# Optimization experiments

Measured on AMD Instinct MI355X. Metric: run time of the kernel, lower is better.

## Reference

```python
import jax, jax.numpy as jnp
import numpy as np

REG_PARAM = 0.0002
COS_EPS = 1e-8  # torch F.cosine_similarity eps


def setup_inputs() -> dict:
    key = jax.random.key(0)
    k1, k2, k3, k4 = jax.random.split(key, 4)
    return {
        "output": jax.random.normal(k1, (32, 3, 256, 256), dtype=jnp.float32),
        "ground_truth": jax.random.normal(k2, (32, 3, 256, 256), dtype=jnp.float32),
        "att": jax.random.normal(k3, (8192, 2000), dtype=jnp.float32),
        "mem": jax.random.normal(k4, (2000, 256), dtype=jnp.float32),
    }


def reference(output, ground_truth, att, mem):
    # MSE reconstruction loss (mean reduction)
    mse = jnp.mean((ground_truth - output) ** 2)

    # Entropy regularizer: sum(softmax * log_softmax) over att, dim=1
    logp = jax.nn.log_softmax(att, axis=1)
    reg = jnp.sum(jnp.exp(logp) * logp)
    loss = mse - REG_PARAM * reg

    # Pairwise cosine-similarity sum over memory vectors:
    # original: nested loop over all i<j pairs; here: normalize + Gram + triu sum
    norms = jnp.maximum(jnp.linalg.norm(mem, axis=1, keepdims=True), COS_EPS)
    unit = mem / norms                      # [N, D]
    gram = unit @ unit.T                    # [N, N]
    cos_sum = jnp.sum(jnp.triu(gram, k=1))  # strict upper triangle = i<j pairs

    return loss + cos_sum
```

## Files before the change

kernel.cpp:

```cpp
#include <hip/hip_runtime.h>
#include <math.h>

#define REG_PARAM 0.0002f
#define COS_EPS 1e-8f

#define MSE_BLOCKS 1024
#define ENT_BLOCKS 1024
#define MEM_BLOCKS 64
#define TOTAL_BLOCKS (MSE_BLOCKS + ENT_BLOCKS + MEM_BLOCKS)

#define WS_MSE  0
#define WS_ENT  1024
#define WS_DIAG 2048
#define WS_COL  2112

__device__ __forceinline__ float waveReduceSum(float v) {
    #pragma unroll
    for (int off = 32; off > 0; off >>= 1)
        v += __shfl_xor(v, off, 64);
    return v;
}

__device__ __forceinline__ float blockReduceSum(float v, float* sh) {
    v = waveReduceSum(v);
    int wid = threadIdx.x >> 6, lane = threadIdx.x & 63;
    __syncthreads();
    if (lane == 0) sh[wid] = v;
    __syncthreads();
    return sh[0] + sh[1] + sh[2] + sh[3];
}

__global__ void partials_kernel(const float4* __restrict__ out4,
                                const float4* __restrict__ gt4,
                                const float4* __restrict__ att4,
                                const float4* __restrict__ mem4,
                                float* __restrict__ ws, int n4) {
    __shared__ float sh[4 * 256];
    __shared__ float shd[4];
    const int b = blockIdx.x;
    const int t = threadIdx.x;
    const int wid = t >> 6, lane = t & 63;

    if (b < MSE_BLOCKS) {
        float acc = 0.f;
        for (int i = b * 256 + t; i < n4; i += MSE_BLOCKS * 256) {
            float4 a = out4[i], g = gt4[i];
            float d0 = g.x - a.x, d1 = g.y - a.y;
            float d2 = g.z - a.z, d3 = g.w - a.w;
            acc += d0 * d0 + d1 * d1 + d2 * d2 + d3 * d3;
        }
        acc = waveReduceSum(acc);
        if (lane == 0) sh[wid] = acc;
        __syncthreads();
        if (t == 0) ws[WS_MSE + b] = sh[0] + sh[1] + sh[2] + sh[3];
    } else if (b < MSE_BLOCKS + ENT_BLOCKS) {
        const int wglobal = (b - MSE_BLOCKS) * 4 + wid;
        float acc = 0.f;
        for (int row = wglobal; row < 8192; row += ENT_BLOCKS * 4) {
            const float4* __restrict__ rp = att4 + (size_t)row * 500;
            float z = 0.f, tt = 0.f;
            #pragma unroll
            for (int k = 0; k < 8; ++k) {
                int idx = lane + (k << 6);
                if (idx < 500) {
                    float4 x = rp[idx];
                    float e;
                    e = __expf(x.x); z += e; tt += x.x * e;
                    e = __expf(x.y); z += e; tt += x.y * e;
                    e = __expf(x.z); z += e; tt += x.z * e;
                    e = __expf(x.w); z += e; tt += x.w * e;
                }
            }
            z = waveReduceSum(z);
            tt = waveReduceSum(tt);
            acc += tt / z - __logf(z);
        }
        if (lane == 0) sh[wid] = acc;
        __syncthreads();
        if (t == 0) ws[WS_ENT + (b - MSE_BLOCKS)] = sh[0] + sh[1] + sh[2] + sh[3];
    } else {
        const int mb = b - MSE_BLOCKS - ENT_BLOCKS;
        const int wglobal = mb * 4 + wid;
        float c0 = 0.f, c1 = 0.f, c2 = 0.f, c3 = 0.f, dacc = 0.f;
        for (int row = wglobal; row < 2000; row += 256) {
            float4 v = mem4[(size_t)row * 64 + lane];
            float ss = v.x * v.x + v.y * v.y + v.z * v.z + v.w * v.w;
            ss = waveReduceSum(ss);
            float inv = 1.f / fmaxf(sqrtf(ss), COS_EPS);
            c0 += v.x * inv; c1 += v.y * inv; c2 += v.z * inv; c3 += v.w * inv;
            if (lane == 0) dacc += ss * inv * inv;
        }
        if (lane == 0) shd[wid] = dacc;
        sh[wid * 256 + lane * 4 + 0] = c0;
        sh[wid * 256 + lane * 4 + 1] = c1;
        sh[wid * 256 + lane * 4 + 2] = c2;
        sh[wid * 256 + lane * 4 + 3] = c3;
        __syncthreads();
        ws[WS_COL + mb * 256 + t] = sh[t] + sh[256 + t] + sh[512 + t] + sh[768 + t];
        if (t == 0) ws[WS_DIAG + mb] = shd[0] + shd[1] + shd[2] + shd[3];
    }
}

__global__ void finalize_kernel(const float* __restrict__ ws,
                                float* __restrict__ out, float inv_n) {
    __shared__ float sh[4];
    const int t = threadIdx.x;

    float v = 0.f;
    #pragma unroll
    for (int k = 0; k < 4; ++k) v += ws[WS_MSE + t + (k << 8)];
    float msesum = blockReduceSum(v, sh);

    v = 0.f;
    #pragma unroll
    for (int k = 0; k < 4; ++k) v += ws[WS_ENT + t + (k << 8)];
    float entsum = blockReduceSum(v, sh);

    float S = 0.f;
    #pragma unroll 8
    for (int b2 = 0; b2 < 64; ++b2) S += ws[WS_COL + (b2 << 8) + t];
    float ssum = blockReduceSum(S * S, sh);

    float dv = (t < 64) ? ws[WS_DIAG + t] : 0.f;
    float diag = blockReduceSum(dv, sh);

    if (t == 0) {
        out[0] = msesum * inv_n - REG_PARAM * entsum + 0.5f * (ssum - diag);
    }
}

extern "C" void kernel_launch(void* const* d_in, const int* in_sizes, int n_in,
                              void* d_out, int out_size, void* d_ws, size_t ws_size,
                              hipStream_t stream) {
    const float* out_img = (const float*)d_in[0];
    const float* gt      = (const float*)d_in[1];
    const float* att     = (const float*)d_in[2];
    const float* mem     = (const float*)d_in[3];
    float* ws = (float*)d_ws;
    float* out = (float*)d_out;

    int n = in_sizes[0];
    int n4 = n / 4;

    partials_kernel<<<TOTAL_BLOCKS, 256, 0, stream>>>(
        (const float4*)out_img, (const float4*)gt,
        (const float4*)att, (const float4*)mem, ws, n4);
    finalize_kernel<<<1, 256, 0, stream>>>(ws, out, 1.0f / (float)n);
}
```

Baseline: 30.50 us.

## Fuse MSE and entropy work into shared blocks, halve memory-norm blocks

Merges the MSE and entropy-regularizer block groups so each of 2048 blocks handles a strided slice of the MSE stream plus exactly one att row per wave, instead of separate block ranges. The memory-normalization section drops from 64 to 32 blocks, and the workspace layout and finalize reduction are adjusted to match. The goal is to balance load across blocks so each one mixes bandwidth-bound MSE loads with exp-heavy entropy work, and to cut the column-partial traffic the finalize kernel reads. The att-row mapping now assumes MAIN_BLOCKS*4 equals 8192 rows exactly.

```diff
diff --git a/kernel.cpp b/kernel.cpp
--- a/kernel.cpp
+++ b/kernel.cpp
@@ -4,15 +4,14 @@
 #define REG_PARAM 0.0002f
 #define COS_EPS 1e-8f
 
-#define MSE_BLOCKS 1024
-#define ENT_BLOCKS 1024
-#define MEM_BLOCKS 64
-#define TOTAL_BLOCKS (MSE_BLOCKS + ENT_BLOCKS + MEM_BLOCKS)
+#define MAIN_BLOCKS 2048
+#define MEM_BLOCKS 32
+#define TOTAL_BLOCKS (MAIN_BLOCKS + MEM_BLOCKS)
 
 #define WS_MSE  0
-#define WS_ENT  1024
-#define WS_DIAG 2048
-#define WS_COL  2112
+#define WS_ENT  2048
+#define WS_DIAG 4096
+#define WS_COL  4352
 
 __device__ __forceinline__ float waveReduceSum(float v) {
     #pragma unroll
@@ -41,9 +40,9 @@
     const int t = threadIdx.x;
     const int wid = t >> 6, lane = t & 63;
 
-    if (b < MSE_BLOCKS) {
+    if (b < MAIN_BLOCKS) {
         float acc = 0.f;
-        for (int i = b * 256 + t; i < n4; i += MSE_BLOCKS * 256) {
+        for (int i = b * 256 + t; i < n4; i += MAIN_BLOCKS * 256) {
             float4 a = out4[i], g = gt4[i];
             float d0 = g.x - a.x, d1 = g.y - a.y;
             float d2 = g.z - a.z, d3 = g.w - a.w;
@@ -51,38 +50,36 @@
         }
         acc = waveReduceSum(acc);
         if (lane == 0) sh[wid] = acc;
+
+        const int row = b * 4 + wid;
+        const float4* __restrict__ rp = att4 + (size_t)row * 500;
+        float z = 0.f, tt = 0.f;
+        #pragma unroll
+        for (int k = 0; k < 8; ++k) {
+            int idx = lane + (k << 6);
+            if (idx < 500) {
+                float4 x = rp[idx];
+                float e;
+                e = __expf(x.x); z += e; tt += x.x * e;
+                e = __expf(x.y); z += e; tt += x.y * e;
+                e = __expf(x.z); z += e; tt += x.z * e;
+                e = __expf(x.w); z += e; tt += x.w * e;
+            }
+        }
+        z = waveReduceSum(z);
+        tt = waveReduceSum(tt);
+        float ent = tt / z - __logf(z);
+        if (lane == 1) sh[4 + wid] = ent;
         __syncthreads();
-        if (t == 0) ws[WS_MSE + b] = sh[0] + sh[1] + sh[2] + sh[3];
-    } else if (b < MSE_BLOCKS + ENT_BLOCKS) {
-        const int wglobal = (b - MSE_BLOCKS) * 4 + wid;
-        float acc = 0.f;
-        for (int row = wglobal; row < 8192; row += ENT_BLOCKS * 4) {
-            const float4* __restrict__ rp = att4 + (size_t)row * 500;
-            float z = 0.f, tt = 0.f;
-            #pragma unroll
-            for (int k = 0; k < 8; ++k) {
-                int idx = lane + (k << 6);
-                if (idx < 500) {
-                    float4 x = rp[idx];
-                    float e;
-                    e = __expf(x.x); z += e; tt += x.x * e;
-                    e = __expf(x.y); z += e; tt += x.y * e;
-                    e = __expf(x.z); z += e; tt += x.z * e;
-                    e = __expf(x.w); z += e; tt += x.w * e;
-                }
-            }
-            z = waveReduceSum(z);
-            tt = waveReduceSum(tt);
-            acc += tt / z - __logf(z);
+        if (t == 0) {
+            ws[WS_MSE + b] = sh[0] + sh[1] + sh[2] + sh[3];
+            ws[WS_ENT + b] = sh[4] + sh[5] + sh[6] + sh[7];
         }
-        if (lane == 0) sh[wid] = acc;
-        __syncthreads();
-        if (t == 0) ws[WS_ENT + (b - MSE_BLOCKS)] = sh[0] + sh[1] + sh[2] + sh[3];
     } else {
-        const int mb = b - MSE_BLOCKS - ENT_BLOCKS;
+        const int mb = b - MAIN_BLOCKS;
         const int wglobal = mb * 4 + wid;
         float c0 = 0.f, c1 = 0.f, c2 = 0.f, c3 = 0.f, dacc = 0.f;
-        for (int row = wglobal; row < 2000; row += 256) {
+        for (int row = wglobal; row < 2000; row += MEM_BLOCKS * 4) {
             float4 v = mem4[(size_t)row * 64 + lane];
             float ss = v.x * v.x + v.y * v.y + v.z * v.z + v.w * v.w;
             ss = waveReduceSum(ss);
@@ -108,20 +105,20 @@
 
     float v = 0.f;
     #pragma unroll
-    for (int k = 0; k < 4; ++k) v += ws[WS_MSE + t + (k << 8)];
+    for (int k = 0; k < 8; ++k) v += ws[WS_MSE + t + (k << 8)];
     float msesum = blockReduceSum(v, sh);
 
     v = 0.f;
     #pragma unroll
-    for (int k = 0; k < 4; ++k) v += ws[WS_ENT + t + (k << 8)];
+    for (int k = 0; k < 8; ++k) v += ws[WS_ENT + t + (k << 8)];
     float entsum = blockReduceSum(v, sh);
 
     float S = 0.f;
-    #pragma unroll 8
-    for (int b2 = 0; b2 < 64; ++b2) S += ws[WS_COL + (b2 << 8) + t];
+    #pragma unroll
+    for (int mb = 0; mb < 32; ++mb) S += ws[WS_COL + (mb << 8) + t];
     float ssum = blockReduceSum(S * S, sh);
 
-    float dv = (t < 64) ? ws[WS_DIAG + t] : 0.f;
+    float dv = (t < 32) ? ws[WS_DIAG + t] : 0.f;
     float diag = blockReduceSum(dv, sh);
 
     if (t == 0) {
```

Measured after the change: 32.27 us. 5.8% more time.
